# Kernel optimization log

Hardware: AMD Instinct MI355X
Metric: run time of the kernel (lower is better)

The kernel has to match this reference:

```python
import jax, jax.numpy as jnp
import numpy as np

EPS = 1e-6
SLOPE = 0.25  # nn.PReLU() default init, recreated each forward -> constant slope


def conv_norm(x, W, b, g, beta):
    # 1x1 conv: [B,C,T,F] x [O,C] -> [B,O,T,F]
    y = jnp.einsum('bctf,oc->botf', x, W) + b[None, :, None, None]
    # GroupNorm(num_groups=1): normalize over (C,T,F) per sample
    mu = jnp.mean(y, axis=(1, 2, 3), keepdims=True)
    var = jnp.var(y, axis=(1, 2, 3), keepdims=True)
    y = (y - mu) * jax.lax.rsqrt(var + EPS)
    y = y * g[None, :, None, None] + beta[None, :, None, None]
    # PReLU with constant slope 0.25
    return jnp.where(y >= 0, y, SLOPE * y)


def setup_inputs() -> dict:
    key = jax.random.key(0)
    ks = jax.random.split(key, 16)
    B, C, T, F = 2, 256, 512, 128
    N, H = 4, 64
    CN = C // N
    f32 = jnp.float32

    def w(k, shape, fan_in):
        return jax.random.normal(k, shape, f32) / np.sqrt(fan_in).astype(np.float32)

    return {
        'x': jax.random.normal(ks[0], (B, C, T, F), f32),
        'Wq': w(ks[1], (N, H, C), C), 'bq': jnp.zeros((N, H), f32),
        'gq': jnp.ones((N, H), f32), 'betaq': jnp.zeros((N, H), f32),
        'Wk': w(ks[2], (N, H, C), C), 'bk': jnp.zeros((N, H), f32),
        'gk': jnp.ones((N, H), f32), 'betak': jnp.zeros((N, H), f32),
        'Wv': w(ks[3], (N, CN, C), C), 'bv': jnp.zeros((N, CN), f32),
        'gv': jnp.ones((N, CN), f32), 'betav': jnp.zeros((N, CN), f32),
        'Wp': w(ks[4], (C, C), C), 'bp': jnp.zeros((C,), f32),
        'gp': jnp.ones((C,), f32), 'betap': jnp.zeros((C,), f32),
    }


def reference(x, Wq, bq, gq, betaq, Wk, bk, gk, betak, Wv, bv, gv, betav,
              Wp, bp, gp, betap):
    B, C, T, F = x.shape
    N = Wq.shape[0]
    CN = C // N

    branch = jax.vmap(conv_norm, in_axes=(None, 0, 0, 0, 0))  # over N heads

    def to_seq(y):
        # [N,B,H,T,F] -> transpose(1,2) in torch -> [N,B,T,H,F] -> flatten(2)
        return jnp.swapaxes(y, 2, 3).reshape(y.shape[0], y.shape[1], y.shape[3], -1)

    Q = to_seq(branch(x, Wq, bq, gq, betaq))  # [N,B,T,H*F]
    K = to_seq(branch(x, Wk, bk, gk, betak))  # [N,B,T,H*F]
    V = to_seq(branch(x, Wv, bv, gv, betav))  # [N,B,T,CN*F]

    scale = 1.0 / np.sqrt(Q.shape[-1]).astype(np.float32)
    attn = jax.nn.softmax(jnp.einsum('nbtd,nbsd->nbts', Q, K) * scale, axis=-1)
    Vo = jnp.einsum('nbts,nbsd->nbtd', attn, V)  # [N,B,T,CN*F]

    # exact replication of the original reshape chain (incl. (f,t) reinterpret)
    Vo = Vo.reshape(N * B, T, CN * F)
    Vo = jnp.swapaxes(Vo, 1, 2)                    # [N*B, CN*F, T]
    Vo = Vo.reshape(N, B, CN, T, F)
    Vo = jnp.swapaxes(Vo, 0, 1).reshape(B, C, T, F)

    out = conv_norm(Vo, Wp, bp, gp, betap)
    return out + x
```

## Files before the change

kernel.cpp:

```cpp
#include <hip/hip_runtime.h>
#include <cstddef>

typedef unsigned short u16;

typedef __bf16 bf16x8 __attribute__((ext_vector_type(8)));
typedef float  f32x4  __attribute__((ext_vector_type(4)));
typedef short  s16x8  __attribute__((ext_vector_type(8)));

__device__ __forceinline__ float us2f(u16 u){
  unsigned int w = ((unsigned int)u) << 16; float f; __builtin_memcpy(&f,&w,4); return f;
}
__device__ __forceinline__ u16 f2us(float f){
  unsigned int u; __builtin_memcpy(&u,&f,4);
  u = (u + 0x7FFFu + ((u>>16)&1u)) >> 16;
  return (u16)u;
}

__device__ __forceinline__ f32x4 mfma16(bf16x8 a, bf16x8 b, f32x4 c){
  return __builtin_amdgcn_mfma_f32_16x16x32_bf16(a, b, c, 0, 0, 0);
}
__device__ __forceinline__ ushort4 pack4(f32x4 a){
  ushort4 p; p.x=f2us(a[0]); p.y=f2us(a[1]); p.z=f2us(a[2]); p.w=f2us(a[3]); return p;
}

constexpr int CC=256, CT=512, CF=128, CD=8192, CTF=65536;
constexpr float EPSV = 1e-6f;
constexpr float SLOPEV = 0.25f;
constexpr float QSCALE = 0.011048543456039806f;

#define OW_Q 0
#define OB_Q 65536
#define OG_Q 65792
#define OBE_Q 66048
#define OW_K 66304
#define OB_K 131840
#define OG_K 132096
#define OBE_K 132352
#define OW_V 132608
#define OB_V 198144
#define OG_V 198400
#define OBE_V 198656
#define OW_P 198912
#define OB_P 264448
#define OG_P 264704
#define OBE_P 264960

__global__ void k_detect(const u16* gq_raw, int* flagp){
  if (threadIdx.x==0 && blockIdx.x==0) *flagp = (gq_raw[0]==0x3F80) ? 1 : 0;
}

__global__ __launch_bounds__(256) void k_prep(
    const void* p1,const void* p2,const void* p3,const void* p4,
    const void* p5,const void* p6,const void* p7,const void* p8,
    const void* p9,const void* p10,const void* p11,const void* p12,
    const void* p13,const void* p14,const void* p15,const void* p16,
    u16* dst, const int* flagp)
{
  const void* src; int size; int off;
  switch(blockIdx.y){
    case  0: src=p1;  size=65536; off=OW_Q;  break;
    case  1: src=p2;  size=256;   off=OB_Q;  break;
    case  2: src=p3;  size=256;   off=OG_Q;  break;
    case  3: src=p4;  size=256;   off=OBE_Q; break;
    case  4: src=p5;  size=65536; off=OW_K;  break;
    case  5: src=p6;  size=256;   off=OB_K;  break;
    case  6: src=p7;  size=256;   off=OG_K;  break;
    case  7: src=p8;  size=256;   off=OBE_K; break;
    case  8: src=p9;  size=65536; off=OW_V;  break;
    case  9: src=p10; size=256;   off=OB_V;  break;
    case 10: src=p11; size=256;   off=OG_V;  break;
    case 11: src=p12; size=256;   off=OBE_V; break;
    case 12: src=p13; size=65536; off=OW_P;  break;
    case 13: src=p14; size=256;   off=OB_P;  break;
    case 14: src=p15; size=256;   off=OG_P;  break;
    default: src=p16; size=256;   off=OBE_P; break;
  }
  int idx = blockIdx.x*256 + threadIdx.x;
  if (idx >= size) return;
  u16 v;
  if (*flagp) v = ((const u16*)src)[idx];
  else        v = f2us(((const float*)src)[idx]);
  dst[off+idx] = v;
}

__global__ __launch_bounds__(256) void k_conv(
    const void* x, const u16* wtsb,
    u16* qn, u16* kn, u16* vn,
    float* stats, const int* flagp, int n, int b0)
{
  const int tid = threadIdx.x;
  const int tf0 = blockIdx.x * 64;
  const int flag = *flagp;

  __shared__ __align__(16) u16 Xs[64][264];
  __shared__ __align__(16) u16 Ys[64][72];
  __shared__ float wred[3][4][2];

  {
    const int tfl = (tid & 31) * 2;
    const int cb  = (tid >> 5) * 4;
    if (flag){
      const u16* xq = (const u16*)x + (size_t)b0*CC*CTF + tf0 + tfl;
      #pragma unroll
      for (int p=0;p<8;p++){
        int c0 = p*32 + cb;
        u16 a0[4], a1[4];
        #pragma unroll
        for (int i=0;i<4;i++){
          ushort2 u = *(const ushort2*)&xq[(size_t)(c0+i)*CTF];
          a0[i]=u.x; a1[i]=u.y;
        }
        *(ushort4*)&Xs[tfl][c0]   = *(const ushort4*)a0;
        *(ushort4*)&Xs[tfl+1][c0] = *(const ushort4*)a1;
      }
    } else {
      const float* xq = (const float*)x + (size_t)b0*CC*CTF + tf0 + tfl;
      #pragma unroll
      for (int p=0;p<8;p++){
        int c0 = p*32 + cb;
        u16 a0[4], a1[4];
        #pragma unroll
        for (int i=0;i<4;i++){
          float2 u = *(const float2*)&xq[(size_t)(c0+i)*CTF];
          a0[i]=f2us(u.x); a1[i]=f2us(u.y);
        }
        *(ushort4*)&Xs[tfl][c0]   = *(const ushort4*)a0;
        *(ushort4*)&Xs[tfl+1][c0] = *(const ushort4*)a1;
      }
    }
  }
  __syncthreads();

  const int l  = tid & 63, w = tid >> 6;
  const int lr = l & 15,  kg = l >> 4;
  const int wy = w >> 1,  wx = w & 1;
  const u16* arow0 = &Xs[wy*32 + lr][8*kg];
  const u16* arow1 = &Xs[wy*32 + 16 + lr][8*kg];
  const int t   = tf0 >> 7;
  const int f0g = tf0 & 127;
  const size_t ybase = (size_t)t*CD + f0g;
  const int o0 = wx*32 + lr;

  for (int br=0; br<3; ++br){
    const u16* W    = wtsb + (br==0?OW_Q: br==1?OW_K:OW_V) + n*64*256;
    const u16* bias = wtsb + (br==0?OB_Q: br==1?OB_K:OB_V) + n*64;
    u16* yo = (br==0? qn : (br==1? kn : vn));
    const u16* bp0 = W + o0*256 + 8*kg;
    const u16* bp1 = bp0 + 16*256;
    float bb0 = us2f(bias[o0]);
    float bb1 = us2f(bias[o0+16]);
    f32x4 acc00 = {bb0,bb0,bb0,bb0};
    f32x4 acc01 = {bb1,bb1,bb1,bb1};
    f32x4 acc10 = {bb0,bb0,bb0,bb0};
    f32x4 acc11 = {bb1,bb1,bb1,bb1};
    #pragma unroll
    for (int d=0; d<256; d+=32){
      bf16x8 a0 = *(const bf16x8*)(arow0 + d);
      bf16x8 a1 = *(const bf16x8*)(arow1 + d);
      bf16x8 b0 = *(const bf16x8*)(bp0 + d);
      bf16x8 b1 = *(const bf16x8*)(bp1 + d);
      acc00 = mfma16(a0,b0,acc00);
      acc01 = mfma16(a0,b1,acc01);
      acc10 = mfma16(a1,b0,acc10);
      acc11 = mfma16(a1,b1,acc11);
    }
    float s=0.f, s2=0.f;
    #pragma unroll
    for (int ii=0; ii<4; ++ii){
      float v;
      v=acc00[ii]; s+=v; s2+=v*v;
      v=acc01[ii]; s+=v; s2+=v*v;
      v=acc10[ii]; s+=v; s2+=v*v;
      v=acc11[ii]; s+=v; s2+=v*v;
    }
    #pragma unroll
    for (int m=1; m<64; m<<=1){ s += __shfl_xor(s,m); s2 += __shfl_xor(s2,m); }
    if (l==0){ wred[br][w][0]=s; wred[br][w][1]=s2; }
    __syncthreads();
    *(ushort4*)&Ys[wx*32 + lr][wy*32 + 4*kg]           = pack4(acc00);
    *(ushort4*)&Ys[wx*32 + 16 + lr][wy*32 + 4*kg]      = pack4(acc01);
    *(ushort4*)&Ys[wx*32 + lr][wy*32 + 16 + 4*kg]      = pack4(acc10);
    *(ushort4*)&Ys[wx*32 + 16 + lr][wy*32 + 16 + 4*kg] = pack4(acc11);
    __syncthreads();
    {
      int oo = tid >> 2, sg = (tid & 3)*16;
      size_t adr = ybase + (size_t)oo*CF + sg;
      *(s16x8*)&yo[adr]     = *(const s16x8*)&Ys[oo][sg];
      *(s16x8*)&yo[adr + 8] = *(const s16x8*)&Ys[oo][sg + 8];
    }
    __syncthreads();
  }
  if (tid < 3){
    float s  = wred[tid][0][0]+wred[tid][1][0]+wred[tid][2][0]+wred[tid][3][0];
    float s2 = wred[tid][0][1]+wred[tid][1][1]+wred[tid][2][1]+wred[tid][3][1];
    int g = tid*8 + n*2 + b0;
    atomicAdd(&stats[2*g],   s);
    atomicAdd(&stats[2*g+1], s2);
  }
}

__global__ __launch_bounds__(256) void k_norm(
    u16* q, u16* k, const u16* wtsb,
    const float* stats, int n, int b0)
{
  const int br = blockIdx.y;
  u16* y = (br==0? q : k);
  const u16* g  = wtsb + (br==0?OG_Q : OG_K ) + n*64;
  const u16* be = wtsb + (br==0?OBE_Q: OBE_K) + n*64;
  size_t idx0 = ((size_t)blockIdx.x*256 + threadIdx.x)*8;
  int ch = (int)((idx0 >> 7) & 63);
  int grp = br*8 + n*2 + b0;
  float sm = stats[2*grp], sq = stats[2*grp+1];
  const float Minv = 1.0f/4194304.0f;
  float mean = sm*Minv;
  float var  = fmaxf(sq*Minv - mean*mean, 0.0f);
  float rs = rsqrtf(var + EPSV);
  float gg = us2f(g[ch]) * rs;
  float bb = us2f(be[ch]);
  float sc = (br==0)? QSCALE : 1.0f;
  ushort4 u0 = *(const ushort4*)&y[idx0];
  ushort4 u1 = *(const ushort4*)&y[idx0+4];
  float vals[8] = {us2f(u0.x),us2f(u0.y),us2f(u0.z),us2f(u0.w),
                   us2f(u1.x),us2f(u1.y),us2f(u1.z),us2f(u1.w)};
  #pragma unroll
  for (int j=0;j<8;j++){
    float t = (vals[j]-mean)*gg + bb;
    t = (t>=0.f)? t : SLOPEV*t;
    vals[j] = t*sc;
  }
  ushort4 o0, o1;
  o0.x=f2us(vals[0]); o0.y=f2us(vals[1]); o0.z=f2us(vals[2]); o0.w=f2us(vals[3]);
  o1.x=f2us(vals[4]); o1.y=f2us(vals[5]); o1.z=f2us(vals[6]); o1.w=f2us(vals[7]);
  *(ushort4*)&y[idx0]   = o0;
  *(ushort4*)&y[idx0+4] = o1;
}

__global__ __launch_bounds__(512) void k_qk(const u16* __restrict__ qm,
                                            const u16* __restrict__ km,
                                            float* __restrict__ S)
{
  const int tid = threadIdx.x;
  const int l   = tid & 63;
  const int w   = tid >> 6;
  const int lr  = l & 15;
  const int kg  = l >> 4;
  const int s0  = blockIdx.x*32;
  const int t0  = blockIdx.y*32;

  const u16* qp = qm + (size_t)(t0 + lr)*CD + w*1024 + 8*kg;
  const u16* kp = km + (size_t)(s0 + lr)*CD + w*1024 + 8*kg;

  f32x4 acc00 = {0.f,0.f,0.f,0.f};
  f32x4 acc01 = acc00, acc10 = acc00, acc11 = acc00;

  #pragma unroll 4
  for (int d=0; d<1024; d+=32){
    bf16x8 a0 = *(const bf16x8*)(qp + d);
    bf16x8 a1 = *(const bf16x8*)(qp + d + 16*CD);
    bf16x8 b0 = *(const bf16x8*)(kp + d);
    bf16x8 b1 = *(const bf16x8*)(kp + d + 16*CD);
    acc00 = mfma16(a0, b0, acc00);
    acc01 = mfma16(a0, b1, acc01);
    acc10 = mfma16(a1, b0, acc10);
    acc11 = mfma16(a1, b1, acc11);
  }

  __shared__ float Sb[8][32][36];
  #pragma unroll
  for (int ii=0; ii<4; ++ii){
    Sb[w][4*kg+ii][lr]       = acc00[ii];
    Sb[w][4*kg+ii][lr+16]    = acc01[ii];
    Sb[w][16+4*kg+ii][lr]    = acc10[ii];
    Sb[w][16+4*kg+ii][lr+16] = acc11[ii];
  }
  __syncthreads();
  #pragma unroll
  for (int rep=0; rep<2; ++rep){
    int idx = tid + rep*512;
    int tt = idx >> 5, ss = idx & 31;
    float v = 0.f;
    #pragma unroll
    for (int ww=0; ww<8; ++ww) v += Sb[ww][tt][ss];
    S[(size_t)(t0+tt)*CT + s0 + ss] = v;
  }
}

__global__ __launch_bounds__(256) void k_vtn(const u16* __restrict__ v,
                                             u16* __restrict__ vt,
                                             const u16* wtsb,
                                             const float* stats, int n, int b0)
{
  __shared__ u16 T[64][72];
  const int tid = threadIdx.x;
  const int d0 = blockIdx.x*64, s0 = blockIdx.y*64;
  {
    int r = tid >> 3, c8 = (tid & 7)*8;
    *(s16x8*)&T[r][c8]    = *(const s16x8*)&v[(size_t)(s0+r)*CD    + d0 + c8];
    *(s16x8*)&T[r+32][c8] = *(const s16x8*)&v[(size_t)(s0+r+32)*CD + d0 + c8];
  }
  __syncthreads();
  int dd = tid >> 2, s16i = (tid & 3)*16;
  int ch = (d0 + dd) >> 7;
  int grp = 16 + n*2 + b0;
  float sm = stats[2*grp], sq = stats[2*grp+1];
  const float Minv = 1.0f/4194304.0f;
  float mean = sm*Minv;
  float var  = fmaxf(sq*Minv - mean*mean, 0.0f);
  float rs = rsqrtf(var + EPSV);
  float gg = us2f(wtsb[OG_V  + n*64 + ch]) * rs;
  float bb = us2f(wtsb[OBE_V + n*64 + ch]);
  u16 tmp[16];
  #pragma unroll
  for (int j=0;j<16;j++){
    float val = us2f(T[s16i+j][dd]);
    float t = (val-mean)*gg + bb;
    t = (t>=0.f)? t : SLOPEV*t;
    tmp[j] = f2us(t);
  }
  *(s16x8*)&vt[(size_t)(d0+dd)*CT + s0 + s16i]     = *(const s16x8*)&tmp[0];
  *(s16x8*)&vt[(size_t)(d0+dd)*CT + s0 + s16i + 8] = *(const s16x8*)&tmp[8];
}

__global__ __launch_bounds__(256) void k_softmax(const float* S, u16* P)
{
  const int row = blockIdx.x;
  const int tid = threadIdx.x;
  const float* Sr = S + (size_t)row*CT;
  u16* Pr = P + (size_t)row*1024;
  float a = Sr[tid], c = Sr[tid+256];
  __shared__ float buf[256];
  float m = fmaxf(a,c);
  buf[tid] = m;
  __syncthreads();
  for (int w=128; w; w>>=1){
    if (tid<w) buf[tid] = fmaxf(buf[tid], buf[tid+w]);
    __syncthreads();
  }
  m = buf[0];
  __syncthreads();
  float e0 = __expf(a-m), e1 = __expf(c-m);
  buf[tid] = e0+e1;
  __syncthreads();
  for (int w=128; w; w>>=1){
    if (tid<w) buf[tid] += buf[tid+w];
    __syncthreads();
  }
  float r = 1.0f/buf[0];
  Pr[tid]     = f2us(e0*r);
  Pr[tid+256] = f2us(e1*r);
}

__global__ __launch_bounds__(256) void k_pv(const u16* __restrict__ P,
                                            const u16* __restrict__ vt,
                                            u16* out_u16, u16* vof_ws,
                                            const int* flagp, int n, int b0)
{
  const int tid = threadIdx.x;
  const int l   = tid & 63;
  const int w   = tid >> 6;
  const int lr  = l & 15;
  const int kg  = l >> 4;
  const int dv0 = blockIdx.x*64;
  const int t00 = blockIdx.y*64;
  const int dvofs = (w >> 1)*32;
  const int tofs  = (w & 1)*32;

  const u16* ap = P  + (size_t)(t00 + tofs + lr)*1024 + 8*kg;
  const u16* bp = vt + (size_t)(dv0 + dvofs + lr)*CT  + 8*kg;

  f32x4 acc00 = {0.f,0.f,0.f,0.f};
  f32x4 acc01 = acc00, acc10 = acc00, acc11 = acc00;

  #pragma unroll 2
  for (int s=0; s<CT; s+=32){
    bf16x8 a0 = *(const bf16x8*)(ap + s);
    bf16x8 a1 = *(const bf16x8*)(ap + s + 16*1024);
    bf16x8 b0 = *(const bf16x8*)(bp + s);
    bf16x8 b1 = *(const bf16x8*)(bp + s + 16*CT);
    acc00 = mfma16(a0, b0, acc00);
    acc01 = mfma16(a0, b1, acc01);
    acc10 = mfma16(a1, b0, acc10);
    acc11 = mfma16(a1, b1, acc11);
  }

  __shared__ __align__(16) u16 Ot[64][72];
  *(ushort4*)&Ot[dvofs + lr][tofs + 4*kg]           = pack4(acc00);
  *(ushort4*)&Ot[dvofs + 16 + lr][tofs + 4*kg]      = pack4(acc01);
  *(ushort4*)&Ot[dvofs + lr][tofs + 16 + 4*kg]      = pack4(acc10);
  *(ushort4*)&Ot[dvofs + 16 + lr][tofs + 16 + 4*kg] = pack4(acc11);
  __syncthreads();

  u16* vof = (*flagp) ? out_u16 : vof_ws;
  {
    int r = tid >> 2, sg = (tid & 3)*16;
    int dv = dv0 + r;
    int cn = dv >> 7, f = dv & 127;
    size_t adr = ((size_t)(b0*CC + n*64 + cn))*CTF + (size_t)f*CT + t00 + sg;
    *(s16x8*)&vof[adr]     = *(const s16x8*)&Ot[r][sg];
    *(s16x8*)&vof[adr + 8] = *(const s16x8*)&Ot[r][sg + 8];
  }
}

__global__ __launch_bounds__(256) void k_proj(u16* out_u16, u16* vof_ws,
                                              const int* flagp,
                                              const u16* wtsb,
                                              float* stats)
{
  const int tid = threadIdx.x;
  const int tf0 = blockIdx.x*64;
  const int b   = blockIdx.y;
  u16* xb = ((*flagp) ? out_u16 : vof_ws) + (size_t)b*CC*CTF;

  __shared__ __align__(16) u16 Xs[64][264];
  __shared__ __align__(16) u16 Yp[64][72];
  __shared__ float wred[4][2];

  {
    const int tfl = (tid & 31) * 2;
    const int cb  = (tid >> 5) * 4;
    const u16* xq = xb + tf0 + tfl;
    #pragma unroll
    for (int p=0;p<8;p++){
      int c0 = p*32 + cb;
      u16 a0[4], a1[4];
      #pragma unroll
      for (int i=0;i<4;i++){
        ushort2 u = *(const ushort2*)&xq[(size_t)(c0+i)*CTF];
        a0[i]=u.x; a1[i]=u.y;
      }
      *(ushort4*)&Xs[tfl][c0]   = *(const ushort4*)a0;
      *(ushort4*)&Xs[tfl+1][c0] = *(const ushort4*)a1;
    }
  }
  __syncthreads();

  const int l  = tid & 63, w = tid >> 6;
  const int lr = l & 15,  kg = l >> 4;
  const int wy = w >> 1,  wx = w & 1;
  const u16* arow0 = &Xs[wy*32 + lr][8*kg];
  const u16* arow1 = &Xs[wy*32 + 16 + lr][8*kg];
  float ts=0.f, ts2=0.f;

  for (int oc=0; oc<4; ++oc){
    const int o0c = oc*64;
    const int o0  = o0c + wx*32 + lr;
    const u16* bp0 = wtsb + OW_P + o0*256 + 8*kg;
    const u16* bp1 = bp0 + 16*256;
    float bb0 = us2f(wtsb[OB_P + o0]);
    float bb1 = us2f(wtsb[OB_P + o0 + 16]);
    f32x4 acc00 = {bb0,bb0,bb0,bb0};
    f32x4 acc01 = {bb1,bb1,bb1,bb1};
    f32x4 acc10 = {bb0,bb0,bb0,bb0};
    f32x4 acc11 = {bb1,bb1,bb1,bb1};
    #pragma unroll
    for (int d=0; d<256; d+=32){
      bf16x8 a0 = *(const bf16x8*)(arow0 + d);
      bf16x8 a1 = *(const bf16x8*)(arow1 + d);
      bf16x8 b0 = *(const bf16x8*)(bp0 + d);
      bf16x8 b1 = *(const bf16x8*)(bp1 + d);
      acc00 = mfma16(a0,b0,acc00);
      acc01 = mfma16(a0,b1,acc01);
      acc10 = mfma16(a1,b0,acc10);
      acc11 = mfma16(a1,b1,acc11);
    }
    #pragma unroll
    for (int ii=0; ii<4; ++ii){
      float v;
      v=acc00[ii]; ts+=v; ts2+=v*v;
      v=acc01[ii]; ts+=v; ts2+=v*v;
      v=acc10[ii]; ts+=v; ts2+=v*v;
      v=acc11[ii]; ts+=v; ts2+=v*v;
    }
    __syncthreads();
    *(ushort4*)&Yp[wx*32 + lr][wy*32 + 4*kg]           = pack4(acc00);
    *(ushort4*)&Yp[wx*32 + 16 + lr][wy*32 + 4*kg]      = pack4(acc01);
    *(ushort4*)&Yp[wx*32 + lr][wy*32 + 16 + 4*kg]      = pack4(acc10);
    *(ushort4*)&Yp[wx*32 + 16 + lr][wy*32 + 16 + 4*kg] = pack4(acc11);
    __syncthreads();
    {
      int ol = tid >> 2, sg = (tid & 3)*16;
      size_t adr = (size_t)(o0c + ol)*CTF + tf0 + sg;
      *(s16x8*)&xb[adr]     = *(const s16x8*)&Yp[ol][sg];
      *(s16x8*)&xb[adr + 8] = *(const s16x8*)&Yp[ol][sg + 8];
    }
    __syncthreads();
  }
  #pragma unroll
  for (int m=1; m<64; m<<=1){ ts += __shfl_xor(ts,m); ts2 += __shfl_xor(ts2,m); }
  if (l==0){ wred[w][0]=ts; wred[w][1]=ts2; }
  __syncthreads();
  if (tid==0){
    float s  = wred[0][0]+wred[1][0]+wred[2][0]+wred[3][0];
    float s2 = wred[0][1]+wred[1][1]+wred[2][1]+wred[3][1];
    atomicAdd(&stats[2*(24+b)],   s);
    atomicAdd(&stats[2*(24+b)+1], s2);
  }
}

__global__ __launch_bounds__(256) void k_final(void* dout, const void* x,
                                               const u16* vof_ws, const int* flagp,
                                               const u16* wtsb,
                                               const float* stats)
{
  const int flag = *flagp;
  size_t idx0 = ((size_t)blockIdx.x*256 + threadIdx.x)*8;
  int b = (int)(idx0 >> 24);
  int c = (int)((idx0 >> 16) & 255);
  float sm = stats[2*(24+b)], sq = stats[2*(24+b)+1];
  const float Minv = 1.0f/16777216.0f;
  float mean = sm*Minv;
  float var  = fmaxf(sq*Minv - mean*mean, 0.0f);
  float rs = rsqrtf(var + EPSV);
  float gg = us2f(wtsb[OG_P + c])*rs, bb = us2f(wtsb[OBE_P + c]);

  const u16* yp = flag ? (const u16*)dout : vof_ws;
  ushort4 u0 = *(const ushort4*)&yp[idx0];
  ushort4 u1 = *(const ushort4*)&yp[idx0+4];
  float vy[8] = {us2f(u0.x),us2f(u0.y),us2f(u0.z),us2f(u0.w),
                 us2f(u1.x),us2f(u1.y),us2f(u1.z),us2f(u1.w)};
  float vx[8];
  if (flag){
    const u16* xb = (const u16*)x;
    ushort4 x0 = *(const ushort4*)&xb[idx0];
    ushort4 x1 = *(const ushort4*)&xb[idx0+4];
    vx[0]=us2f(x0.x); vx[1]=us2f(x0.y); vx[2]=us2f(x0.z); vx[3]=us2f(x0.w);
    vx[4]=us2f(x1.x); vx[5]=us2f(x1.y); vx[6]=us2f(x1.z); vx[7]=us2f(x1.w);
  } else {
    const float* xf = (const float*)x;
    float4 x0 = *(const float4*)&xf[idx0];
    float4 x1 = *(const float4*)&xf[idx0+4];
    vx[0]=x0.x; vx[1]=x0.y; vx[2]=x0.z; vx[3]=x0.w;
    vx[4]=x1.x; vx[5]=x1.y; vx[6]=x1.z; vx[7]=x1.w;
  }
  #pragma unroll
  for (int j=0;j<8;j++){
    float t = (vy[j]-mean)*gg + bb;
    t = (t>=0.f)? t : SLOPEV*t;
    vy[j] = t + vx[j];
  }
  if (flag){
    u16* ob = (u16*)dout;
    ushort4 o0, o1;
    o0.x=f2us(vy[0]); o0.y=f2us(vy[1]); o0.z=f2us(vy[2]); o0.w=f2us(vy[3]);
    o1.x=f2us(vy[4]); o1.y=f2us(vy[5]); o1.z=f2us(vy[6]); o1.w=f2us(vy[7]);
    *(ushort4*)&ob[idx0]   = o0;
    *(ushort4*)&ob[idx0+4] = o1;
  } else {
    float* of = (float*)dout;
    *(float4*)&of[idx0]   = make_float4(vy[0],vy[1],vy[2],vy[3]);
    *(float4*)&of[idx0+4] = make_float4(vy[4],vy[5],vy[6],vy[7]);
  }
}

extern "C" void kernel_launch(void* const* d_in, const int* in_sizes, int n_in,
                              void* d_out, int out_size, void* d_ws, size_t ws_size,
                              hipStream_t stream)
{
  (void)in_sizes; (void)n_in; (void)out_size; (void)ws_size;
  char* ws = (char*)d_ws;
  int* flagp    = (int*)ws;
  float* stats  = (float*)(ws + 16);
  u16* wtsb     = (u16*)(ws + 512);
  u16* qn       = (u16*)(ws + 532480);
  u16* kn       = (u16*)(ws + 8921088);
  u16* vn       = (u16*)(ws + 17309696);
  float* Sn     = (float*)(ws + 25698304);
  u16* vof_ws   = (u16*)(ws + 27262976);
  u16* out_u16  = (u16*)d_out;

  hipMemsetAsync(stats, 0, 256, stream);
  k_detect<<<1,64,0,stream>>>((const u16*)d_in[3], flagp);
  k_prep<<<dim3(256,16),256,0,stream>>>(d_in[1],d_in[2],d_in[3],d_in[4],
                                        d_in[5],d_in[6],d_in[7],d_in[8],
                                        d_in[9],d_in[10],d_in[11],d_in[12],
                                        d_in[13],d_in[14],d_in[15],d_in[16],
                                        wtsb, flagp);
  for (int n=0; n<4; ++n){
    for (int b0=0; b0<2; ++b0){
      k_conv<<<dim3(1024),256,0,stream>>>(d_in[0], wtsb, qn,kn,vn, stats, flagp, n, b0);
      k_norm<<<dim3(2048,2),256,0,stream>>>(qn,kn, wtsb, stats, n, b0);
      k_qk<<<dim3(16,16),512,0,stream>>>(qn,kn,Sn);
      k_vtn<<<dim3(128,8),256,0,stream>>>(vn, qn, wtsb, stats, n, b0);
      k_softmax<<<512,256,0,stream>>>(Sn,(u16*)Sn);
      k_pv<<<dim3(128,8),256,0,stream>>>((const u16*)Sn, qn, out_u16, vof_ws, flagp, n, b0);
    }
  }
  k_proj<<<dim3(1024,2),256,0,stream>>>(out_u16, vof_ws, flagp, wtsb, stats);
  k_final<<<16384,256,0,stream>>>(d_out, d_in[0], vof_ws, flagp, wtsb, stats);
}
```

Before: 1.525 ms.

## Pre-transpose activations and enlarge GEMM tiles in conv, PV, projection kernels

Adds a transpose kernel that writes x (and later the attention output) in channel-contiguous bf16 layout. The conv and projection GEMMs can then load MFMA A fragments directly from global memory instead of staging a strided gather through shared memory. The conv input transpose runs once per batch rather than once per head. The PV and projection kernels use larger per-wave tiles (4x4 MFMA blocks), the V transpose uses 128x128 tiles, and the loop order becomes batch-outer. This trades extra transpose passes and workspace-buffer juggling for better data reuse and fewer, larger blocks, which may lower occupancy through higher register use.

```diff
diff --git a/kernel.cpp b/kernel.cpp
--- a/kernel.cpp
+++ b/kernel.cpp
@@ -83,113 +83,129 @@
   dst[off+idx] = v;
 }
 
+__global__ __launch_bounds__(256) void k_xt(const void* xin, u16* out_u16, u16* vof_ws,
+                                            const int* flagp, int which, int b)
+{
+  const int tid = threadIdx.x;
+  const int tf0 = blockIdx.x*128, c0 = blockIdx.y*128;
+  const int flag = *flagp;
+  __shared__ __align__(16) u16 Ts[128*136];
+
+  if (which==0){
+    const int c = tid>>1, h = tid&1;
+    if (flag){
+      const u16* src = (const u16*)xin + ((size_t)b<<24);
+      #pragma unroll
+      for (int j=0;j<8;j++){
+        int tc = h*64 + j*8;
+        *(s16x8*)&Ts[c*136 + tc] = *(const s16x8*)&src[(size_t)(c0+c)*CTF + tf0 + tc];
+      }
+    } else {
+      const float* src = (const float*)xin + ((size_t)b<<24);
+      #pragma unroll
+      for (int j=0;j<8;j++){
+        int tc = h*64 + j*8;
+        float4 u0 = *(const float4*)&src[(size_t)(c0+c)*CTF + tf0 + tc];
+        float4 u1 = *(const float4*)&src[(size_t)(c0+c)*CTF + tf0 + tc + 4];
+        u16 tmp[8] = {f2us(u0.x),f2us(u0.y),f2us(u0.z),f2us(u0.w),
+                      f2us(u1.x),f2us(u1.y),f2us(u1.z),f2us(u1.w)};
+        *(s16x8*)&Ts[c*136 + tc] = *(const s16x8*)tmp;
+      }
+    }
+  } else {
+    const u16* src = (flag ? out_u16 : vof_ws) + ((size_t)b<<24);
+    const int c = tid>>1, h = tid&1;
+    #pragma unroll
+    for (int j=0;j<8;j++){
+      int tc = h*64 + j*8;
+      *(s16x8*)&Ts[c*136 + tc] = *(const s16x8*)&src[(size_t)(c0+c)*CTF + tf0 + tc];
+    }
+  }
+  __syncthreads();
+
+  u16* dst;
+  if (which==0) dst = flag ? vof_ws : (out_u16 + ((size_t)1<<25));
+  else          dst = (flag ? vof_ws : out_u16) + ((size_t)b<<24);
+
+  const int d = tid>>1, h2 = tid&1;
+  #pragma unroll
+  for (int j=0;j<8;j++){
+    int sc = h2*64 + j*8;
+    u16 tmp[8];
+    #pragma unroll
+    for (int i=0;i<8;i++) tmp[i] = Ts[(sc+i)*136 + d];
+    *(s16x8*)&dst[(size_t)(tf0 + d)*256 + c0 + sc] = *(const s16x8*)tmp;
+  }
+}
+
 __global__ __launch_bounds__(256) void k_conv(
-    const void* x, const u16* wtsb,
+    const u16* xt_a, const u16* xt_b, const u16* wtsb,
     u16* qn, u16* kn, u16* vn,
     float* stats, const int* flagp, int n, int b0)
 {
   const int tid = threadIdx.x;
-  const int tf0 = blockIdx.x * 64;
-  const int flag = *flagp;
-
-  __shared__ __align__(16) u16 Xs[64][264];
-  __shared__ __align__(16) u16 Ys[64][72];
+  const int t   = blockIdx.x;
+  const u16* xt = (*flagp) ? xt_a : xt_b;
+
+  const int l = tid & 63, w = tid >> 6;
+  const int lr = l & 15, kg = l >> 4;
+
+  __shared__ __align__(16) u16 Ys[64*136];
   __shared__ float wred[3][4][2];
 
-  {
-    const int tfl = (tid & 31) * 2;
-    const int cb  = (tid >> 5) * 4;
-    if (flag){
-      const u16* xq = (const u16*)x + (size_t)b0*CC*CTF + tf0 + tfl;
-      #pragma unroll
-      for (int p=0;p<8;p++){
-        int c0 = p*32 + cb;
-        u16 a0[4], a1[4];
-        #pragma unroll
-        for (int i=0;i<4;i++){
-          ushort2 u = *(const ushort2*)&xq[(size_t)(c0+i)*CTF];
-          a0[i]=u.x; a1[i]=u.y;
-        }
-        *(ushort4*)&Xs[tfl][c0]   = *(const ushort4*)a0;
-        *(ushort4*)&Xs[tfl+1][c0] = *(const ushort4*)a1;
-      }
-    } else {
-      const float* xq = (const float*)x + (size_t)b0*CC*CTF + tf0 + tfl;
-      #pragma unroll
-      for (int p=0;p<8;p++){
-        int c0 = p*32 + cb;
-        u16 a0[4], a1[4];
-        #pragma unroll
-        for (int i=0;i<4;i++){
-          float2 u = *(const float2*)&xq[(size_t)(c0+i)*CTF];
-          a0[i]=f2us(u.x); a1[i]=f2us(u.y);
-        }
-        *(ushort4*)&Xs[tfl][c0]   = *(const ushort4*)a0;
-        *(ushort4*)&Xs[tfl+1][c0] = *(const ushort4*)a1;
-      }
-    }
-  }
-  __syncthreads();
-
-  const int l  = tid & 63, w = tid >> 6;
-  const int lr = l & 15,  kg = l >> 4;
-  const int wy = w >> 1,  wx = w & 1;
-  const u16* arow0 = &Xs[wy*32 + lr][8*kg];
-  const u16* arow1 = &Xs[wy*32 + 16 + lr][8*kg];
-  const int t   = tf0 >> 7;
-  const int f0g = tf0 & 127;
-  const size_t ybase = (size_t)t*CD + f0g;
-  const int o0 = wx*32 + lr;
+  bf16x8 a[2][8];
+  #pragma unroll
+  for (int i=0;i<2;i++){
+    const u16* ar = xt + (size_t)(t*128 + w*32 + i*16 + lr)*256 + 8*kg;
+    #pragma unroll
+    for (int d=0;d<8;d++) a[i][d] = *(const bf16x8*)(ar + d*32);
+  }
 
   for (int br=0; br<3; ++br){
     const u16* W    = wtsb + (br==0?OW_Q: br==1?OW_K:OW_V) + n*64*256;
     const u16* bias = wtsb + (br==0?OB_Q: br==1?OB_K:OB_V) + n*64;
     u16* yo = (br==0? qn : (br==1? kn : vn));
-    const u16* bp0 = W + o0*256 + 8*kg;
-    const u16* bp1 = bp0 + 16*256;
-    float bb0 = us2f(bias[o0]);
-    float bb1 = us2f(bias[o0+16]);
-    f32x4 acc00 = {bb0,bb0,bb0,bb0};
-    f32x4 acc01 = {bb1,bb1,bb1,bb1};
-    f32x4 acc10 = {bb0,bb0,bb0,bb0};
-    f32x4 acc11 = {bb1,bb1,bb1,bb1};
-    #pragma unroll
-    for (int d=0; d<256; d+=32){
-      bf16x8 a0 = *(const bf16x8*)(arow0 + d);
-      bf16x8 a1 = *(const bf16x8*)(arow1 + d);
-      bf16x8 b0 = *(const bf16x8*)(bp0 + d);
-      bf16x8 b1 = *(const bf16x8*)(bp1 + d);
-      acc00 = mfma16(a0,b0,acc00);
-      acc01 = mfma16(a0,b1,acc01);
-      acc10 = mfma16(a1,b0,acc10);
-      acc11 = mfma16(a1,b1,acc11);
+    f32x4 acc[2][4];
+    #pragma unroll
+    for (int j=0;j<4;j++){
+      float bb = us2f(bias[j*16+lr]);
+      acc[0][j] = (f32x4){bb,bb,bb,bb};
+      acc[1][j] = (f32x4){bb,bb,bb,bb};
+    }
+    #pragma unroll
+    for (int d=0; d<8; ++d){
+      #pragma unroll
+      for (int j=0;j<4;j++){
+        bf16x8 bfr = *(const bf16x8*)(W + (size_t)(j*16+lr)*256 + 8*kg + d*32);
+        acc[0][j] = mfma16(a[0][d], bfr, acc[0][j]);
+        acc[1][j] = mfma16(a[1][d], bfr, acc[1][j]);
+      }
     }
     float s=0.f, s2=0.f;
     #pragma unroll
-    for (int ii=0; ii<4; ++ii){
-      float v;
-      v=acc00[ii]; s+=v; s2+=v*v;
-      v=acc01[ii]; s+=v; s2+=v*v;
-      v=acc10[ii]; s+=v; s2+=v*v;
-      v=acc11[ii]; s+=v; s2+=v*v;
-    }
+    for (int i=0;i<2;i++)
+      #pragma unroll
+      for (int j=0;j<4;j++)
+        #pragma unroll
+        for (int ii=0;ii<4;ii++){ float v = acc[i][j][ii]; s += v; s2 += v*v; }
     #pragma unroll
     for (int m=1; m<64; m<<=1){ s += __shfl_xor(s,m); s2 += __shfl_xor(s2,m); }
     if (l==0){ wred[br][w][0]=s; wred[br][w][1]=s2; }
     __syncthreads();
-    *(ushort4*)&Ys[wx*32 + lr][wy*32 + 4*kg]           = pack4(acc00);
-    *(ushort4*)&Ys[wx*32 + 16 + lr][wy*32 + 4*kg]      = pack4(acc01);
-    *(ushort4*)&Ys[wx*32 + lr][wy*32 + 16 + 4*kg]      = pack4(acc10);
-    *(ushort4*)&Ys[wx*32 + 16 + lr][wy*32 + 16 + 4*kg] = pack4(acc11);
+    #pragma unroll
+    for (int i=0;i<2;i++)
+      #pragma unroll
+      for (int j=0;j<4;j++)
+        *(ushort4*)&Ys[(j*16+lr)*136 + (w*32 + i*16 + 4*kg)] = pack4(acc[i][j]);
     __syncthreads();
-    {
-      int oo = tid >> 2, sg = (tid & 3)*16;
-      size_t adr = ybase + (size_t)oo*CF + sg;
-      *(s16x8*)&yo[adr]     = *(const s16x8*)&Ys[oo][sg];
-      *(s16x8*)&yo[adr + 8] = *(const s16x8*)&Ys[oo][sg + 8];
-    }
-    __syncthreads();
-  }
+    #pragma unroll
+    for (int k2=0;k2<4;k2++){
+      int idx = tid + k2*256;
+      int o = idx >> 4, f8 = (idx & 15)*8;
+      *(s16x8*)&yo[(size_t)t*CD + o*CF + f8] = *(const s16x8*)&Ys[o*136 + f8];
+    }
+  }
+  __syncthreads();
   if (tid < 3){
     float s  = wred[tid][0][0]+wred[tid][1][0]+wred[tid][2][0]+wred[tid][3][0];
     float s2 = wred[tid][0][1]+wred[tid][1][1]+wred[tid][2][1]+wred[tid][3][1];
@@ -290,18 +306,21 @@
                                              const u16* wtsb,
                                              const float* stats, int n, int b0)
 {
-  __shared__ u16 T[64][72];
-  const int tid = threadIdx.x;
-  const int d0 = blockIdx.x*64, s0 = blockIdx.y*64;
+  const int tid = threadIdx.x;
+  const int d0 = blockIdx.x*128, s0 = blockIdx.y*128;
+  __shared__ __align__(16) u16 Ts[128*136];
   {
-    int r = tid >> 3, c8 = (tid & 7)*8;
-    *(s16x8*)&T[r][c8]    = *(const s16x8*)&v[(size_t)(s0+r)*CD    + d0 + c8];
-    *(s16x8*)&T[r+32][c8] = *(const s16x8*)&v[(size_t)(s0+r+32)*CD + d0 + c8];
-  }
-  __syncthreads();
-  int dd = tid >> 2, s16i = (tid & 3)*16;
-  int ch = (d0 + dd) >> 7;
-  int grp = 16 + n*2 + b0;
+    const int sA = tid>>1, h = tid&1;
+    #pragma unroll
+    for (int j=0;j<8;j++){
+      int dc = h*64 + j*8;
+      *(s16x8*)&Ts[sA*136 + dc] = *(const s16x8*)&v[(size_t)(s0+sA)*CD + d0 + dc];
+    }
+  }
+  __syncthreads();
+  const int dl = tid>>1, h2 = tid&1;
+  const int ch = (d0 + dl) >> 7;
+  const int grp = 16 + n*2 + b0;
   float sm = stats[2*grp], sq = stats[2*grp+1];
   const float Minv = 1.0f/4194304.0f;
   float mean = sm*Minv;
@@ -309,16 +328,19 @@
   float rs = rsqrtf(var + EPSV);
   float gg = us2f(wtsb[OG_V  + n*64 + ch]) * rs;
   float bb = us2f(wtsb[OBE_V + n*64 + ch]);
-  u16 tmp[16];
-  #pragma unroll
-  for (int j=0;j<16;j++){
-    float val = us2f(T[s16i+j][dd]);
-    float t = (val-mean)*gg + bb;
-    t = (t>=0.f)? t : SLOPEV*t;
-    tmp[j] = f2us(t);
-  }
-  *(s16x8*)&vt[(size_t)(d0+dd)*CT + s0 + s16i]     = *(const s16x8*)&tmp[0];
-  *(s16x8*)&vt[(size_t)(d0+dd)*CT + s0 + s16i + 8] = *(const s16x8*)&tmp[8];
+  #pragma unroll
+  for (int j=0;j<8;j++){
+    int sc = h2*64 + j*8;
+    u16 tmp[8];
+    #pragma unroll
+    for (int i=0;i<8;i++){
+      float val = us2f(Ts[(sc+i)*136 + dl]);
+      float t = (val-mean)*gg + bb;
+      t = (t>=0.f)? t : SLOPEV*t;
+      tmp[i] = f2us(t);
+    }
+    *(s16x8*)&vt[(size_t)(d0+dl)*CT + s0 + sc] = *(const s16x8*)tmp;
+  }
 }
 
 __global__ __launch_bounds__(256) void k_softmax(const float* S, u16* P)
@@ -356,48 +378,50 @@
                                             const int* flagp, int n, int b0)
 {
   const int tid = threadIdx.x;
-  const int l   = tid & 63;
-  const int w   = tid >> 6;
-  const int lr  = l & 15;
-  const int kg  = l >> 4;
+  const int l = tid & 63, w = tid >> 6;
+  const int lr = l & 15, kg = l >> 4;
   const int dv0 = blockIdx.x*64;
-  const int t00 = blockIdx.y*64;
-  const int dvofs = (w >> 1)*32;
-  const int tofs  = (w & 1)*32;
-
-  const u16* ap = P  + (size_t)(t00 + tofs + lr)*1024 + 8*kg;
-  const u16* bp = vt + (size_t)(dv0 + dvofs + lr)*CT  + 8*kg;
-
-  f32x4 acc00 = {0.f,0.f,0.f,0.f};
-  f32x4 acc01 = acc00, acc10 = acc00, acc11 = acc00;
-
-  #pragma unroll 2
+  const int t00 = blockIdx.y*256;
+  const int tb  = t00 + w*64;
+
+  const u16* ap0 = P  + (size_t)(tb + lr)*1024 + 8*kg;
+  const u16* bp0 = vt + (size_t)(dv0 + lr)*CT  + 8*kg;
+
+  f32x4 acc[4][4];
+  #pragma unroll
+  for (int i=0;i<4;i++)
+    #pragma unroll
+    for (int j=0;j<4;j++) acc[i][j] = (f32x4){0.f,0.f,0.f,0.f};
+
   for (int s=0; s<CT; s+=32){
-    bf16x8 a0 = *(const bf16x8*)(ap + s);
-    bf16x8 a1 = *(const bf16x8*)(ap + s + 16*1024);
-    bf16x8 b0 = *(const bf16x8*)(bp + s);
-    bf16x8 b1 = *(const bf16x8*)(bp + s + 16*CT);
-    acc00 = mfma16(a0, b0, acc00);
-    acc01 = mfma16(a0, b1, acc01);
-    acc10 = mfma16(a1, b0, acc10);
-    acc11 = mfma16(a1, b1, acc11);
-  }
-
-  __shared__ __align__(16) u16 Ot[64][72];
-  *(ushort4*)&Ot[dvofs + lr][tofs + 4*kg]           = pack4(acc00);
-  *(ushort4*)&Ot[dvofs + 16 + lr][tofs + 4*kg]      = pack4(acc01);
-  *(ushort4*)&Ot[dvofs + lr][tofs + 16 + 4*kg]      = pack4(acc10);
-  *(ushort4*)&Ot[dvofs + 16 + lr][tofs + 16 + 4*kg] = pack4(acc11);
+    bf16x8 av[4], bv[4];
+    #pragma unroll
+    for (int i=0;i<4;i++) av[i] = *(const bf16x8*)(ap0 + (size_t)i*16*1024 + s);
+    #pragma unroll
+    for (int j=0;j<4;j++) bv[j] = *(const bf16x8*)(bp0 + (size_t)j*16*CT + s);
+    #pragma unroll
+    for (int i=0;i<4;i++)
+      #pragma unroll
+      for (int j=0;j<4;j++)
+        acc[i][j] = mfma16(av[i], bv[j], acc[i][j]);
+  }
+
+  __shared__ __align__(16) u16 Ot[64*264];
+  #pragma unroll
+  for (int i=0;i<4;i++)
+    #pragma unroll
+    for (int j=0;j<4;j++)
+      *(ushort4*)&Ot[(j*16+lr)*264 + (w*64 + i*16 + 4*kg)] = pack4(acc[i][j]);
   __syncthreads();
 
   u16* vof = (*flagp) ? out_u16 : vof_ws;
-  {
-    int r = tid >> 2, sg = (tid & 3)*16;
-    int dv = dv0 + r;
-    int cn = dv >> 7, f = dv & 127;
-    size_t adr = ((size_t)(b0*CC + n*64 + cn))*CTF + (size_t)f*CT + t00 + sg;
-    *(s16x8*)&vof[adr]     = *(const s16x8*)&Ot[r][sg];
-    *(s16x8*)&vof[adr + 8] = *(const s16x8*)&Ot[r][sg + 8];
+  #pragma unroll
+  for (int k2=0;k2<8;k2++){
+    int idx = tid + k2*256;
+    int r = idx >> 5, t8 = (idx & 31)*8;
+    int dv = dv0 + r, cn = dv >> 7, f = dv & 127;
+    *(s16x8*)&vof[((size_t)(b0*CC + n*64 + cn))*CTF + (size_t)f*CT + t00 + t8] =
+        *(const s16x8*)&Ot[r*264 + t8];
   }
 }
 
@@ -407,91 +431,66 @@
                                               float* stats)
 {
   const int tid = threadIdx.x;
-  const int tf0 = blockIdx.x*64;
+  const int tf0 = blockIdx.x*256;
   const int b   = blockIdx.y;
-  u16* xb = ((*flagp) ? out_u16 : vof_ws) + (size_t)b*CC*CTF;
-
-  __shared__ __align__(16) u16 Xs[64][264];
-  __shared__ __align__(16) u16 Yp[64][72];
-  __shared__ float wred[4][2];
-
-  {
-    const int tfl = (tid & 31) * 2;
-    const int cb  = (tid >> 5) * 4;
-    const u16* xq = xb + tf0 + tfl;
-    #pragma unroll
-    for (int p=0;p<8;p++){
-      int c0 = p*32 + cb;
-      u16 a0[4], a1[4];
-      #pragma unroll
-      for (int i=0;i<4;i++){
-        ushort2 u = *(const ushort2*)&xq[(size_t)(c0+i)*CTF];
-        a0[i]=u.x; a1[i]=u.y;
-      }
-      *(ushort4*)&Xs[tfl][c0]   = *(const ushort4*)a0;
-      *(ushort4*)&Xs[tfl+1][c0] = *(const ushort4*)a1;
-    }
-  }
-  __syncthreads();
-
-  const int l  = tid & 63, w = tid >> 6;
-  const int lr = l & 15,  kg = l >> 4;
-  const int wy = w >> 1,  wx = w & 1;
-  const u16* arow0 = &Xs[wy*32 + lr][8*kg];
-  const u16* arow1 = &Xs[wy*32 + 16 + lr][8*kg];
+  const int flag = *flagp;
+  const u16* vtT = (flag ? vof_ws : out_u16) + ((size_t)b<<24);
+  u16* yb        = (flag ? out_u16 : vof_ws) + ((size_t)b<<24);
+
+  __shared__ __align__(16) u16 Ys[64*264];
+  __shared__ float wredp[4][2];
+  const int l = tid&63, w = tid>>6, lr = l&15, kg = l>>4;
   float ts=0.f, ts2=0.f;
 
   for (int oc=0; oc<4; ++oc){
     const int o0c = oc*64;
-    const int o0  = o0c + wx*32 + lr;
-    const u16* bp0 = wtsb + OW_P + o0*256 + 8*kg;
-    const u16* bp1 = bp0 + 16*256;
-    float bb0 = us2f(wtsb[OB_P + o0]);
-    float bb1 = us2f(wtsb[OB_P + o0 + 16]);
-    f32x4 acc00 = {bb0,bb0,bb0,bb0};
-    f32x4 acc01 = {bb1,bb1,bb1,bb1};
-    f32x4 acc10 = {bb0,bb0,bb0,bb0};
-    f32x4 acc11 = {bb1,bb1,bb1,bb1};
-    #pragma unroll
-    for (int d=0; d<256; d+=32){
-      bf16x8 a0 = *(const bf16x8*)(arow0 + d);
-      bf16x8 a1 = *(const bf16x8*)(arow1 + d);
-      bf16x8 b0 = *(const bf16x8*)(bp0 + d);
-      bf16x8 b1 = *(const bf16x8*)(bp1 + d);
-      acc00 = mfma16(a0,b0,acc00);
-      acc01 = mfma16(a0,b1,acc01);
-      acc10 = mfma16(a1,b0,acc10);
-      acc11 = mfma16(a1,b1,acc11);
-    }
-    #pragma unroll
-    for (int ii=0; ii<4; ++ii){
-      float v;
-      v=acc00[ii]; ts+=v; ts2+=v*v;
-      v=acc01[ii]; ts+=v; ts2+=v*v;
-      v=acc10[ii]; ts+=v; ts2+=v*v;
-      v=acc11[ii]; ts+=v; ts2+=v*v;
-    }
+    f32x4 acc[4][4];
+    #pragma unroll
+    for (int j=0;j<4;j++){
+      float bb = us2f(wtsb[OB_P + o0c + j*16 + lr]);
+      #pragma unroll
+      for (int i=0;i<4;i++) acc[i][j] = (f32x4){bb,bb,bb,bb};
+    }
+    #pragma unroll
+    for (int d=0; d<8; ++d){
+      bf16x8 av[4];
+      #pragma unroll
+      for (int i=0;i<4;i++)
+        av[i] = *(const bf16x8*)(vtT + (size_t)(tf0 + w*64 + i*16 + lr)*256 + 8*kg + d*32);
+      #pragma unroll
+      for (int j=0;j<4;j++){
+        bf16x8 bfr = *(const bf16x8*)(wtsb + OW_P + (size_t)(o0c + j*16 + lr)*256 + 8*kg + d*32);
+        #pragma unroll
+        for (int i=0;i<4;i++) acc[i][j] = mfma16(av[i], bfr, acc[i][j]);
+      }
+    }
+    #pragma unroll
+    for (int i=0;i<4;i++)
+      #pragma unroll
+      for (int j=0;j<4;j++)
+        #pragma unroll
+        for (int ii=0;ii<4;ii++){ float v = acc[i][j][ii]; ts += v; ts2 += v*v; }
     __syncthreads();
-    *(ushort4*)&Yp[wx*32 + lr][wy*32 + 4*kg]           = pack4(acc00);
-    *(ushort4*)&Yp[wx*32 + 16 + lr][wy*32 + 4*kg]      = pack4(acc01);
-    *(ushort4*)&Yp[wx*32 + lr][wy*32 + 16 + 4*kg]      = pack4(acc10);
-    *(ushort4*)&Yp[wx*32 + 16 + lr][wy*32 + 16 + 4*kg] = pack4(acc11);
+    #pragma unroll
+    for (int i=0;i<4;i++)
+      #pragma unroll
+      for (int j=0;j<4;j++)
+        *(ushort4*)&Ys[(j*16+lr)*264 + (w*64 + i*16 + 4*kg)] = pack4(acc[i][j]);
     __syncthreads();
-    {
-      int ol = tid >> 2, sg = (tid & 3)*16;
-      size_t adr = (size_t)(o0c + ol)*CTF + tf0 + sg;
-      *(s16x8*)&xb[adr]     = *(const s16x8*)&Yp[ol][sg];
-      *(s16x8*)&xb[adr + 8] = *(const s16x8*)&Yp[ol][sg + 8];
-    }
-    __syncthreads();
+    #pragma unroll
+    for (int k2=0;k2<8;k2++){
+      int idx = tid + k2*256;
+      int o = idx >> 5, t8 = (idx & 31)*8;
+      *(s16x8*)&yb[(size_t)(o0c + o)*CTF + tf0 + t8] = *(const s16x8*)&Ys[o*264 + t8];
+    }
   }
   #pragma unroll
   for (int m=1; m<64; m<<=1){ ts += __shfl_xor(ts,m); ts2 += __shfl_xor(ts2,m); }
-  if (l==0){ wred[w][0]=ts; wred[w][1]=ts2; }
+  if (l==0){ wredp[w][0]=ts; wredp[w][1]=ts2; }
   __syncthreads();
   if (tid==0){
-    float s  = wred[0][0]+wred[1][0]+wred[2][0]+wred[3][0];
-    float s2 = wred[0][1]+wred[1][1]+wred[2][1]+wred[3][1];
+    float s  = wredp[0][0]+wredp[1][0]+wredp[2][0]+wredp[3][0];
+    float s2 = wredp[0][1]+wredp[1][1]+wredp[2][1]+wredp[3][1];
     atomicAdd(&stats[2*(24+b)],   s);
     atomicAdd(&stats[2*(24+b)+1], s2);
   }
@@ -575,16 +574,20 @@
                                         d_in[9],d_in[10],d_in[11],d_in[12],
                                         d_in[13],d_in[14],d_in[15],d_in[16],
                                         wtsb, flagp);
-  for (int n=0; n<4; ++n){
-    for (int b0=0; b0<2; ++b0){
-      k_conv<<<dim3(1024),256,0,stream>>>(d_in[0], wtsb, qn,kn,vn, stats, flagp, n, b0);
+  for (int b0=0; b0<2; ++b0){
+    k_xt<<<dim3(512,2),256,0,stream>>>(d_in[0], out_u16, vof_ws, flagp, 0, b0);
+    for (int n=0; n<4; ++n){
+      k_conv<<<512,256,0,stream>>>(vof_ws, out_u16 + ((size_t)1<<25), wtsb,
+                                   qn,kn,vn, stats, flagp, n, b0);
       k_norm<<<dim3(2048,2),256,0,stream>>>(qn,kn, wtsb, stats, n, b0);
       k_qk<<<dim3(16,16),512,0,stream>>>(qn,kn,Sn);
-      k_vtn<<<dim3(128,8),256,0,stream>>>(vn, qn, wtsb, stats, n, b0);
+      k_vtn<<<dim3(64,4),256,0,stream>>>(vn, qn, wtsb, stats, n, b0);
       k_softmax<<<512,256,0,stream>>>(Sn,(u16*)Sn);
-      k_pv<<<dim3(128,8),256,0,stream>>>((const u16*)Sn, qn, out_u16, vof_ws, flagp, n, b0);
-    }
-  }
-  k_proj<<<dim3(1024,2),256,0,stream>>>(out_u16, vof_ws, flagp, wtsb, stats);
+      k_pv<<<dim3(128,2),256,0,stream>>>((const u16*)Sn, qn, out_u16, vof_ws, flagp, n, b0);
+    }
+  }
+  k_xt<<<dim3(512,2),256,0,stream>>>(d_in[0], out_u16, vof_ws, flagp, 1, 0);
+  k_xt<<<dim3(512,2),256,0,stream>>>(d_in[0], out_u16, vof_ws, flagp, 1, 1);
+  k_proj<<<dim3(256,2),256,0,stream>>>(out_u16, vof_ws, flagp, wtsb, stats);
   k_final<<<16384,256,0,stream>>>(d_out, d_in[0], vof_ws, flagp, wtsb, stats);
 }
```

Result: faster. 1.398 ms (-8.3%).
